# Optimization experiments

Hardware: AMD Instinct MI355X
Metric: run time of the kernel (lower is better)

The kernel has to match this reference:

```python
import jax, jax.numpy as jnp
import numpy as np

N_NODES = 50000
N_EDGES = 1000000


def _edge_conv(x, src, dst, W, b, n_nodes):
    """PyG EdgeConv: msg = nn(cat([x_i, x_j - x_i])), aggr=max over incoming edges."""
    xi = x[dst]                      # [E, C] target features
    xj = x[src]                      # [E, C] source features
    m = jnp.concatenate([xi, xj - xi], axis=-1)          # [E, 2C]
    m = jax.nn.relu(m @ W + b)                           # [E, C_out]
    out = jax.ops.segment_max(m, dst, num_segments=n_nodes)  # [N, C_out]
    # empty segments produce -inf; PyG fills with 0
    return jnp.where(jnp.isfinite(out), out, 0.0)


def setup_inputs() -> dict:
    key = jax.random.key(0)
    ks = jax.random.split(key, 12)
    x = jax.random.normal(ks[0], (N_NODES, 3), dtype=jnp.float32)
    edge_index = jax.random.randint(ks[1], (2, N_EDGES), 0, N_NODES, dtype=jnp.int64)

    def lin(k, fan_in, fan_out):
        s = 1.0 / np.sqrt(fan_in)
        kw, kb = jax.random.split(k)
        W = jax.random.uniform(kw, (fan_in, fan_out), jnp.float32, -s, s)
        b = jax.random.uniform(kb, (fan_out,), jnp.float32, -s, s)
        return W, b

    W1, b1 = lin(ks[2], 6, 64)       # conv1 MLP([3*2, 64])
    W2, b2 = lin(ks[3], 128, 128)    # conv2 MLP([64*2, 128])
    W3, b3 = lin(ks[4], 256, 512)    # conv3 MLP([128*2, 512])
    W4, b4 = lin(ks[5], 512, 256)    # lin1 MLP([512, 256])
    W5, b5 = lin(ks[6], 256, 3)      # lin1 final Linear(256, 3)
    return {"x": x, "edge_index": edge_index,
            "W1": W1, "b1": b1, "W2": W2, "b2": b2, "W3": W3, "b3": b3,
            "W4": W4, "b4": b4, "W5": W5, "b5": b5}


def reference(x, edge_index, W1, b1, W2, b2, W3, b3, W4, b4, W5, b5):
    src = edge_index[0]  # x_j
    dst = edge_index[1]  # x_i (aggregation target)
    n = x.shape[0]
    x1 = _edge_conv(x, src, dst, W1, b1, n)    # [N, 64]
    x2 = _edge_conv(x1, src, dst, W2, b2, n)   # [N, 128]
    x3 = _edge_conv(x2, src, dst, W3, b3, n)   # [N, 512]
    x4 = jax.nn.relu(x3 @ W4 + b4) @ W5 + b5   # [N, 3]
    return x + x4
```

## Files before the change

kernel.cpp:

```cpp
#include <hip/hip_runtime.h>

static constexpr int NN = 50000;
static constexpr int NE = 1000000;

typedef short bf16x8 __attribute__((ext_vector_type(8)));
typedef float f32x4 __attribute__((ext_vector_type(4)));
typedef unsigned short u16x2 __attribute__((ext_vector_type(2)));

__device__ inline float bf2f_raw(unsigned short u) {
    return __uint_as_float(((unsigned int)u) << 16);
}
__device__ inline unsigned short f2bf(float f) {
    unsigned int u = __float_as_uint(f);
    u += 0x7fffu + ((u >> 16) & 1u);
    return (unsigned short)(u >> 16);
}
__device__ inline unsigned short f2bfs(float f) {
    unsigned short b = f2bf(f);
    return (b & 0x8000u) ? (unsigned short)(~b) : (unsigned short)(b | 0x8000u);
}
__device__ inline float unsrt2f(unsigned short v) {
    unsigned short b = (v & 0x8000u) ? (unsigned short)(v ^ 0x8000u)
                                     : (unsigned short)(~v);
    return bf2f_raw(b);
}
__device__ inline unsigned int pkmax(unsigned int a, unsigned int b) {
    u16x2 r = __builtin_elementwise_max(__builtin_bit_cast(u16x2, a),
                                        __builtin_bit_cast(u16x2, b));
    return __builtin_bit_cast(unsigned int, r);
}
__device__ inline uint4 pkmax4(uint4 a, uint4 b) {
    a.x = pkmax(a.x, b.x); a.y = pkmax(a.y, b.y);
    a.z = pkmax(a.z, b.z); a.w = pkmax(a.w, b.w);
    return a;
}
__device__ inline unsigned int pack2(float f0, float f1) {
    return (unsigned int)f2bf(f0) | ((unsigned int)f2bf(f1) << 16);
}
__device__ inline unsigned int addrelu2t(unsigned int a, unsigned int t) {
    float t0 = unsrt2f((unsigned short)(t & 0xffffu));
    float t1 = unsrt2f((unsigned short)(t >> 16));
    float f0 = fmaxf(bf2f_raw((unsigned short)(a & 0xffffu)) + t0, 0.f);
    float f1 = fmaxf(bf2f_raw((unsigned short)(a >> 16)) + t1, 0.f);
    return pack2(f0, f1);
}


__global__ void setup_kernel(const float* __restrict__ x, const float* __restrict__ W1,
                             const float* __restrict__ b1, const float* __restrict__ b5,
                             const float* __restrict__ W2, const float* __restrict__ W3,
                             const float* __restrict__ W4,
                             unsigned short* __restrict__ as1, float* __restrict__ out,
                             int* __restrict__ deg, int* __restrict__ cursor,
                             unsigned short* __restrict__ Bt2,
                             unsigned short* __restrict__ Bt3,
                             unsigned short* __restrict__ W4t) {
    int t = blockIdx.x * blockDim.x + threadIdx.x;
    if (t < NN * 128) {
        int i = t >> 7, c = t & 127;
        float x0 = x[i * 3 + 0], x1 = x[i * 3 + 1], x2 = x[i * 3 + 2];
        if (c < 64) {
            float v = x0 * (W1[c] - W1[192 + c]) + x1 * (W1[64 + c] - W1[256 + c]) +
                      x2 * (W1[128 + c] - W1[320 + c]) + b1[c];
            as1[t] = f2bf(v);
        } else {
            int cs = c - 64;
            float v = x0 * W1[192 + cs] + x1 * W1[256 + cs] + x2 * W1[320 + cs];
            as1[t] = f2bfs(v);
        }
        return;
    }
    t -= NN * 128;
    if (t < NN * 3) { out[t] = x[t] + b5[t % 3]; return; }
    t -= NN * 3;
    if (t < NN) { deg[t] = 0; return; }
    t -= NN;
    if (t < NN) { cursor[t] = 0; return; }
    t -= NN;
    if (t < 8192) {
        int k = t / 128, c = t % 128;
        float wt = W2[k * 128 + c];
        float wb = W2[(64 + k) * 128 + c];
        Bt2[c * 64 + k] = f2bf(wt - wb);
        Bt2[(128 + c) * 64 + k] = f2bf(wb);
        return;
    }
    t -= 8192;
    if (t < 65536) {
        int k = t / 512, c = t % 512;
        float wt = W3[k * 512 + c];
        float wb = W3[(128 + k) * 512 + c];
        Bt3[c * 128 + k] = f2bf(wt - wb);
        Bt3[(512 + c) * 128 + k] = f2bf(wb);
        return;
    }
    t -= 65536;
    if (t < 131072) {
        int k = t / 256, n = t % 256;
        W4t[n * 512 + k] = f2bf(W4[k * 256 + n]);
    }
}


__global__ void hist_kernel(const int* __restrict__ dst, int* __restrict__ deg) {
    int e = blockIdx.x * blockDim.x + threadIdx.x;
    if (e < NE) atomicAdd(&deg[dst[e]], 1);
}

__global__ __launch_bounds__(1024) void scan_kernel(const int* __restrict__ deg,
                                                    int* __restrict__ rowstart) {
    __shared__ int wave_sums[16];
    constexpr int CH = (NN + 1023) / 1024;
    int tid = threadIdx.x;
    int lane = tid & 63;
    int wave = tid >> 6;
    int base = tid * CH;
    int vals[CH];
    int sum = 0;
    #pragma unroll
    for (int i = 0; i < CH; ++i) {
        int idx = base + i;
        vals[i] = (idx < NN) ? deg[idx] : 0;
        sum += vals[i];
    }
    int x = sum;
    #pragma unroll
    for (int off = 1; off < 64; off <<= 1) {
        int y = __shfl_up(x, off);
        if (lane >= off) x += y;
    }
    if (lane == 63) wave_sums[wave] = x;
    __syncthreads();
    if (wave == 0 && lane < 16) {
        int s = wave_sums[lane];
        #pragma unroll
        for (int off = 1; off < 16; off <<= 1) {
            int y = __shfl_up(s, off);
            if (lane >= off) s += y;
        }
        wave_sums[lane] = s;
    }
    __syncthreads();
    int run = (wave ? wave_sums[wave - 1] : 0) + x - sum;
    #pragma unroll
    for (int i = 0; i < CH; ++i) {
        int idx = base + i;
        if (idx < NN) rowstart[idx] = run;
        run += vals[i];
    }
    if (tid == 1023) rowstart[NN] = run;
}

__global__ void scatter_kernel(const int* __restrict__ src, const int* __restrict__ dst,
                               const int* __restrict__ rowstart, int* __restrict__ cursor,
                               int* __restrict__ csr) {
    int e = blockIdx.x * blockDim.x + threadIdx.x;
    if (e < NE) {
        int d = dst[e];
        int pos = atomicAdd(&cursor[d], 1);
        csr[rowstart[d] + pos] = src[e];
    }
}


__global__ __launch_bounds__(256) void edge_fused_conv1_kernel(
    const unsigned short* __restrict__ as, const int* __restrict__ rowstart,
    const int* __restrict__ csr, unsigned short* __restrict__ x1) {
    int wid = (blockIdx.x * 256 + threadIdx.x) >> 6;
    int lane = threadIdx.x & 63;
    if (wid >= NN) return;
    int e0 = __builtin_amdgcn_readfirstlane(rowstart[wid]);
    int e1 = __builtin_amdgcn_readfirstlane(rowstart[wid + 1]);
    int nedge = e1 - e0;
    unsigned int mA = 0u, mB = 0u;
    if (nedge > 0) {
        int last = nedge - 1;
        for (int e = 0; e < nedge; e += 16) {
            int jj[16];
            #pragma unroll
            for (int k = 0; k < 16; ++k) {
                int idx = e + k; if (idx > last) idx = last;
                jj[k] = __builtin_amdgcn_readfirstlane(csr[e0 + idx]);
            }
            unsigned int v[16];
            #pragma unroll
            for (int k = 0; k < 16; ++k)
                v[k] = *(const unsigned short*)(as + (size_t)jj[k] * 128 + 64 + lane);
            #pragma unroll
            for (int k = 0; k < 16; ++k) {
                if (k & 1) mB = mB > v[k] ? mB : v[k];
                else       mA = mA > v[k] ? mA : v[k];
            }
        }
    }
    unsigned int m = mA > mB ? mA : mB;
    unsigned short a = as[(size_t)wid * 128 + lane];
    float t = unsrt2f((unsigned short)m);
    float f = fmaxf(bf2f_raw(a) + t, 0.f);
    x1[(size_t)wid * 64 + lane] = f2bf(f);
}


__global__ __launch_bounds__(256) void edge_fused128_kernel(
    const unsigned short* __restrict__ as, const int* __restrict__ rowstart,
    const int* __restrict__ csr, unsigned short* __restrict__ xout) {
    int wid = (blockIdx.x * 256 + threadIdx.x) >> 6;
    int lane = threadIdx.x & 63;
    if (wid >= NN) return;
    int e0 = __builtin_amdgcn_readfirstlane(rowstart[wid]);
    int e1 = __builtin_amdgcn_readfirstlane(rowstart[wid + 1]);
    int nedge = e1 - e0;
    unsigned int mA = 0u, mB = 0u;
    if (nedge > 0) {
        int last = nedge - 1;
        for (int e = 0; e < nedge; e += 16) {
            int jj[16];
            #pragma unroll
            for (int k = 0; k < 16; ++k) {
                int idx = e + k; if (idx > last) idx = last;
                jj[k] = __builtin_amdgcn_readfirstlane(csr[e0 + idx]);
            }
            unsigned int v[16];
            #pragma unroll
            for (int k = 0; k < 16; ++k)
                v[k] = *(const unsigned int*)(as + (size_t)jj[k] * 256 + 128 + lane * 2);
            #pragma unroll
            for (int k = 0; k < 16; ++k) {
                if (k & 1) mB = pkmax(mB, v[k]);
                else       mA = pkmax(mA, v[k]);
            }
        }
    }
    unsigned int t = pkmax(mA, mB);
    unsigned int av = *(const unsigned int*)(as + (size_t)wid * 256 + lane * 2);
    *(unsigned int*)(xout + (size_t)wid * 128 + lane * 2) = addrelu2t(av, t);
}


__global__ __launch_bounds__(256) void ef512_w5_kernel(
    const unsigned short* __restrict__ s3, const unsigned short* __restrict__ x2,
    const int* __restrict__ rowstart, const int* __restrict__ csr,
    const unsigned short* __restrict__ Bt3a, const float* __restrict__ b3,
    const unsigned short* __restrict__ W4t,
    const float* __restrict__ b4, const float* __restrict__ W5,
    float* __restrict__ out) {
    __shared__ __align__(16) unsigned short X[16][520];
    __shared__ __align__(16) unsigned short x2t[16][136];
    int tid = threadIdx.x;
    int wave = tid >> 6, lane = tid & 63;
    int quad = lane >> 4, l16 = lane & 15;
    int tilebase = blockIdx.x * 16;

    {
        int row = tid >> 4, seg = tid & 15;
        uint4 v = *(const uint4*)(x2 + (size_t)(tilebase + row) * 128 + seg * 8);
        *(uint4*)&x2t[row][seg * 8] = v;
    }
    __syncthreads();

    {
        int colbase = wave * 128;
        f32x4 acc3[8] = {};
        #pragma unroll
        for (int kc = 0; kc < 4; ++kc) {
            bf16x8 afr = *(const bf16x8*)&x2t[l16][kc * 32 + quad * 8];
            #pragma unroll
            for (int nt = 0; nt < 8; ++nt) {
                int col = colbase + nt * 16 + l16;
                bf16x8 bfr = *(const bf16x8*)&Bt3a[(size_t)col * 128 + kc * 32 + quad * 8];
                acc3[nt] = __builtin_amdgcn_mfma_f32_16x16x32_bf16(afr, bfr, acc3[nt], 0, 0, 0);
            }
        }
        #pragma unroll
        for (int nt = 0; nt < 8; ++nt) {
            int col = colbase + nt * 16 + l16;
            float bv = b3[col];
            #pragma unroll
            for (int r = 0; r < 4; ++r)
                X[quad * 4 + r][col] = f2bf(acc3[nt][r] + bv);
        }
    }
    __syncthreads();

    const unsigned short* sb = s3 + (size_t)lane * 8;
    for (int i = 0; i < 4; ++i) {
        int node = tilebase + wave * 4 + i;
        int e0 = __builtin_amdgcn_readfirstlane(rowstart[node]);
        int e1 = __builtin_amdgcn_readfirstlane(rowstart[node + 1]);
        int nedge = e1 - e0;
        uint4 mA = make_uint4(0u, 0u, 0u, 0u), mB = make_uint4(0u, 0u, 0u, 0u);
        if (nedge > 0) {
            int last = nedge - 1;
            for (int e = 0; e < nedge; e += 8) {
                int jj[8];
                #pragma unroll
                for (int k = 0; k < 8; ++k) {
                    int idx = e + k; if (idx > last) idx = last;
                    jj[k] = __builtin_amdgcn_readfirstlane(csr[e0 + idx]);
                }
                uint4 v[8];
                #pragma unroll
                for (int k = 0; k < 8; ++k)
                    v[k] = *(const uint4*)(sb + (size_t)jj[k] * 512);
                #pragma unroll
                for (int k = 0; k < 8; ++k) {
                    if (k & 1) mB = pkmax4(mB, v[k]);
                    else       mA = pkmax4(mA, v[k]);
                }
            }
        }
        uint4 m = pkmax4(mA, mB);
        uint4 av = *(const uint4*)&X[wave * 4 + i][lane * 8];
        uint4 o;
        o.x = addrelu2t(av.x, m.x);
        o.y = addrelu2t(av.y, m.y);
        o.z = addrelu2t(av.z, m.z);
        o.w = addrelu2t(av.w, m.w);
        *(uint4*)&X[wave * 4 + i][lane * 8] = o;
    }
    __syncthreads();

    int colbase = wave * 64;
    f32x4 acc4[4] = {};
    for (int kc = 0; kc < 16; ++kc) {
        bf16x8 afr = *(const bf16x8*)&X[l16][kc * 32 + quad * 8];
        #pragma unroll
        for (int nt = 0; nt < 4; ++nt) {
            int col = colbase + nt * 16 + l16;
            bf16x8 bfr = *(const bf16x8*)&W4t[(size_t)col * 512 + kc * 32 + quad * 8];
            acc4[nt] = __builtin_amdgcn_mfma_f32_16x16x32_bf16(afr, bfr, acc4[nt], 0, 0, 0);
        }
    }
    float b4v[4], w5r[4][3];
    #pragma unroll
    for (int nt = 0; nt < 4; ++nt) {
        int col = colbase + nt * 16 + l16;
        b4v[nt] = b4[col];
        w5r[nt][0] = W5[col * 3 + 0];
        w5r[nt][1] = W5[col * 3 + 1];
        w5r[nt][2] = W5[col * 3 + 2];
    }
    #pragma unroll
    for (int r = 0; r < 4; ++r) {
        int row = tilebase + quad * 4 + r;
        float p0 = 0.f, p1 = 0.f, p2 = 0.f;
        #pragma unroll
        for (int nt = 0; nt < 4; ++nt) {
            float h = fmaxf(acc4[nt][r] + b4v[nt], 0.f);
            p0 += h * w5r[nt][0];
            p1 += h * w5r[nt][1];
            p2 += h * w5r[nt][2];
        }
        #pragma unroll
        for (int m = 8; m; m >>= 1) {
            p0 += __shfl_xor(p0, m);
            p1 += __shfl_xor(p1, m);
            p2 += __shfl_xor(p2, m);
        }
        if (l16 == 0) {
            atomicAdd(&out[row * 3 + 0], p0);
            atomicAdd(&out[row * 3 + 1], p1);
            atomicAdd(&out[row * 3 + 2], p2);
        }
    }
}


template<int K, int NT>
__global__ __launch_bounds__(256) void mfma_gemm_nloop_kernel(
    const unsigned short* __restrict__ A, const unsigned short* __restrict__ Bt,
    const float* __restrict__ bias, int bias_n,
    unsigned short* __restrict__ C, int M) {
    constexpr int KC = K / 32;
    constexpr int N = NT * 128;
    __shared__ __align__(16) unsigned short Asl[KC][128 * 40];
    __shared__ __align__(16) unsigned short Bsl[128 * 40];
    int tid = threadIdx.x;
    int mbase = blockIdx.x * 128;
    int wave = tid >> 6, lane = tid & 63;
    int wm = (wave >> 1) * 64, wn = (wave & 1) * 64;
    int quad = lane >> 4, l16 = lane & 15;

    #pragma unroll
    for (int c = tid; c < KC * 512; c += 256) {
        int kc = c >> 9, rem = c & 511;
        int r = rem >> 2, kk = (rem & 3) * 8;
        uint4 va = make_uint4(0u, 0u, 0u, 0u);
        int gr = mbase + r;
        if (gr < M) va = *(const uint4*)&A[(size_t)gr * K + kc * 32 + kk];
        *(uint4*)&Asl[kc][r * 40 + kk] = va;
    }

    for (int nt = 0; nt < NT; ++nt) {
        int nbase = nt * 128;
        f32x4 acc[4][4] = {};
        for (int kc = 0; kc < KC; ++kc) {
            __syncthreads();
            #pragma unroll
            for (int h = 0; h < 2; ++h) {
                int c = tid + h * 256;
                int r = c >> 2, kk = (c & 3) * 8;
                uint4 vb = *(const uint4*)&Bt[(size_t)(nbase + r) * K + kc * 32 + kk];
                *(uint4*)&Bsl[r * 40 + kk] = vb;
            }
            __syncthreads();
            bf16x8 af[4], bfr[4];
            #pragma unroll
            for (int tt = 0; tt < 4; ++tt) {
                af[tt]  = *(const bf16x8*)&Asl[kc][(wm + tt * 16 + l16) * 40 + quad * 8];
                bfr[tt] = *(const bf16x8*)&Bsl[(wn + tt * 16 + l16) * 40 + quad * 8];
            }
            #pragma unroll
            for (int mt = 0; mt < 4; ++mt)
                #pragma unroll
                for (int ntt = 0; ntt < 4; ++ntt)
                    acc[mt][ntt] = __builtin_amdgcn_mfma_f32_16x16x32_bf16(
                        af[mt], bfr[ntt], acc[mt][ntt], 0, 0, 0);
        }
        #pragma unroll
        for (int mt = 0; mt < 4; ++mt) {
            #pragma unroll
            for (int r = 0; r < 4; ++r) {
                int row = mbase + wm + mt * 16 + quad * 4 + r;
                if (row >= M) continue;
                #pragma unroll
                for (int ntt = 0; ntt < 4; ++ntt) {
                    int col = nbase + wn + ntt * 16 + l16;
                    float v = acc[mt][ntt][r];
                    unsigned short o;
                    if (col < bias_n) o = f2bf(v + bias[col]);
                    else o = f2bfs(v);
                    C[(size_t)row * N + col] = o;
                }
            }
        }
    }
}

__global__ void fallback_copy_kernel(const float* __restrict__ x, float* __restrict__ out) {
    int t = blockIdx.x * blockDim.x + threadIdx.x;
    if (t < NN * 3) out[t] = x[t];
}


extern "C" void kernel_launch(void* const* d_in, const int* in_sizes, int n_in,
                              void* d_out, int out_size, void* d_ws, size_t ws_size,
                              hipStream_t stream) {
    const float* x  = (const float*)d_in[0];
    const int*   ei = (const int*)d_in[1];
    const float* W1 = (const float*)d_in[2];
    const float* b1 = (const float*)d_in[3];
    const float* W2 = (const float*)d_in[4];
    const float* b2 = (const float*)d_in[5];
    const float* W3 = (const float*)d_in[6];
    const float* b3 = (const float*)d_in[7];
    const float* W4 = (const float*)d_in[8];
    const float* b4 = (const float*)d_in[9];
    const float* W5 = (const float*)d_in[10];
    const float* b5 = (const float*)d_in[11];
    float* out = (float*)d_out;

    char* p = (char*)d_ws;
    auto alloc = [&](size_t bytes) -> void* {
        void* r = (void*)p;
        p += (bytes + 255) & ~(size_t)255;
        return r;
    };
    int* deg      = (int*)alloc((size_t)NN * 4);
    int* rowstart = (int*)alloc((size_t)(NN + 1) * 4);
    int* cursor   = (int*)alloc((size_t)NN * 4);
    int* csr      = (int*)alloc((size_t)NE * 4);
    unsigned short* Bt2 = (unsigned short*)alloc(256 * 64 * 2);
    unsigned short* Bt3 = (unsigned short*)alloc(1024 * 128 * 2);
    unsigned short* W4t = (unsigned short*)alloc(256 * 512 * 2);
    unsigned short* x1 = (unsigned short*)alloc((size_t)NN * 64 * 2);
    unsigned short* x2 = (unsigned short*)alloc((size_t)NN * 128 * 2);
    unsigned short* as_slab = (unsigned short*)alloc((size_t)NN * 512 * 2);
    size_t need = (size_t)(p - (char*)d_ws);
    if (ws_size < need) {
        fallback_copy_kernel<<<(NN * 3 + 255) / 256, 256, 0, stream>>>(x, out);
        return;
    }

    const int* src = ei;
    const int* dst = ei + NE;

    constexpr int SETUP_T = NN * 128 + NN * 3 + NN + NN + 8192 + 65536 + 131072;
    setup_kernel<<<(SETUP_T + 255) / 256, 256, 0, stream>>>(
        x, W1, b1, b5, W2, W3, W4, as_slab, out, deg, cursor, Bt2, Bt3, W4t);

    hist_kernel<<<(NE + 255) / 256, 256, 0, stream>>>(dst, deg);
    scan_kernel<<<1, 1024, 0, stream>>>(deg, rowstart);
    scatter_kernel<<<(NE + 255) / 256, 256, 0, stream>>>(src, dst, rowstart, cursor, csr);

    edge_fused_conv1_kernel<<<12500, 256, 0, stream>>>(as_slab, rowstart, csr, x1);

    mfma_gemm_nloop_kernel<64, 2><<<391, 256, 0, stream>>>(
        x1, Bt2, b2, 128, as_slab, NN);
    edge_fused128_kernel<<<12500, 256, 0, stream>>>(as_slab, rowstart, csr, x2);

    mfma_gemm_nloop_kernel<128, 4><<<391, 256, 0, stream>>>(
        x2, Bt3 + 512 * 128, b3, 0, as_slab, NN);

    ef512_w5_kernel<<<NN / 16, 256, 0, stream>>>(
        as_slab, x2, rowstart, csr, Bt3, b3, W4t, b4, W5, out);
}
```

Measured before the change: 580.3 us.

## Fuse conv2 self-term GEMM into edge max kernel and reorder conv3 tile work

The conv2 GEMM now computes only the neighbour half (128 columns) into a compact slab. The per-node self term (x1·W_a + b) is computed inside a new tiled edge-max kernel with MFMA on a 16-node tile, so the slab stride for the gathered neighbour rows drops from 256 to 128 shorts. In the conv3 kernel the gather/max runs before the self-term MFMA, with the A fragments preloaded from shared memory, so gather latency and MFMA work can overlap across waves. This trades a smaller gathered slab and less GEMM output traffic for extra per-block MFMA work and registers holding the max results.

```diff
diff --git a/kernel.cpp b/kernel.cpp
--- a/kernel.cpp
+++ b/kernel.cpp
@@ -201,39 +201,86 @@
 }
 
 
-__global__ __launch_bounds__(256) void edge_fused128_kernel(
-    const unsigned short* __restrict__ as, const int* __restrict__ rowstart,
-    const int* __restrict__ csr, unsigned short* __restrict__ xout) {
-    int wid = (blockIdx.x * 256 + threadIdx.x) >> 6;
-    int lane = threadIdx.x & 63;
-    if (wid >= NN) return;
-    int e0 = __builtin_amdgcn_readfirstlane(rowstart[wid]);
-    int e1 = __builtin_amdgcn_readfirstlane(rowstart[wid + 1]);
-    int nedge = e1 - e0;
-    unsigned int mA = 0u, mB = 0u;
-    if (nedge > 0) {
-        int last = nedge - 1;
-        for (int e = 0; e < nedge; e += 16) {
-            int jj[16];
-            #pragma unroll
-            for (int k = 0; k < 16; ++k) {
-                int idx = e + k; if (idx > last) idx = last;
-                jj[k] = __builtin_amdgcn_readfirstlane(csr[e0 + idx]);
-            }
-            unsigned int v[16];
-            #pragma unroll
-            for (int k = 0; k < 16; ++k)
-                v[k] = *(const unsigned int*)(as + (size_t)jj[k] * 256 + 128 + lane * 2);
-            #pragma unroll
-            for (int k = 0; k < 16; ++k) {
-                if (k & 1) mB = pkmax(mB, v[k]);
-                else       mA = pkmax(mA, v[k]);
-            }
-        }
-    }
-    unsigned int t = pkmax(mA, mB);
-    unsigned int av = *(const unsigned int*)(as + (size_t)wid * 256 + lane * 2);
-    *(unsigned int*)(xout + (size_t)wid * 128 + lane * 2) = addrelu2t(av, t);
+__global__ __launch_bounds__(256) void ef128_a2_kernel(
+    const unsigned short* __restrict__ s2, const unsigned short* __restrict__ x1,
+    const int* __restrict__ rowstart, const int* __restrict__ csr,
+    const unsigned short* __restrict__ Bt2a, const float* __restrict__ b2,
+    unsigned short* __restrict__ x2) {
+    __shared__ __align__(16) unsigned short x1t[16][72];
+    __shared__ __align__(16) unsigned short A2[16][136];
+    int tid = threadIdx.x;
+    int wave = tid >> 6, lane = tid & 63;
+    int quad = lane >> 4, l16 = lane & 15;
+    int tilebase = blockIdx.x * 16;
+
+    if (tid < 128) {
+        int row = tid >> 3, seg = tid & 7;
+        uint4 v = *(const uint4*)(x1 + (size_t)(tilebase + row) * 64 + seg * 8);
+        *(uint4*)&x1t[row][seg * 8] = v;
+    }
+    __syncthreads();
+
+    unsigned int m[4];
+    for (int i = 0; i < 4; ++i) {
+        int node = tilebase + wave * 4 + i;
+        int e0 = __builtin_amdgcn_readfirstlane(rowstart[node]);
+        int e1 = __builtin_amdgcn_readfirstlane(rowstart[node + 1]);
+        int nedge = e1 - e0;
+        unsigned int mA = 0u, mB = 0u;
+        if (nedge > 0) {
+            int last = nedge - 1;
+            for (int e = 0; e < nedge; e += 16) {
+                int jj[16];
+                #pragma unroll
+                for (int k = 0; k < 16; ++k) {
+                    int idx = e + k; if (idx > last) idx = last;
+                    jj[k] = __builtin_amdgcn_readfirstlane(csr[e0 + idx]);
+                }
+                unsigned int v[16];
+                #pragma unroll
+                for (int k = 0; k < 16; ++k)
+                    v[k] = *(const unsigned int*)(s2 + (size_t)jj[k] * 128 + lane * 2);
+                #pragma unroll
+                for (int k = 0; k < 16; ++k) {
+                    if (k & 1) mB = pkmax(mB, v[k]);
+                    else       mA = pkmax(mA, v[k]);
+                }
+            }
+        }
+        m[i] = pkmax(mA, mB);
+    }
+
+    {
+        int colbase = wave * 32;
+        f32x4 acc[2] = {};
+        #pragma unroll
+        for (int kc = 0; kc < 2; ++kc) {
+            bf16x8 afr = *(const bf16x8*)&x1t[l16][kc * 32 + quad * 8];
+            #pragma unroll
+            for (int nt = 0; nt < 2; ++nt) {
+                int col = colbase + nt * 16 + l16;
+                bf16x8 bfr = *(const bf16x8*)&Bt2a[(size_t)col * 64 + kc * 32 + quad * 8];
+                acc[nt] = __builtin_amdgcn_mfma_f32_16x16x32_bf16(afr, bfr, acc[nt], 0, 0, 0);
+            }
+        }
+        #pragma unroll
+        for (int nt = 0; nt < 2; ++nt) {
+            int col = colbase + nt * 16 + l16;
+            float bv = b2[col];
+            #pragma unroll
+            for (int r = 0; r < 4; ++r)
+                A2[quad * 4 + r][col] = f2bf(acc[nt][r] + bv);
+        }
+    }
+    __syncthreads();
+
+    #pragma unroll
+    for (int i = 0; i < 4; ++i) {
+        int row = wave * 4 + i;
+        unsigned int av = *(const unsigned int*)&A2[row][lane * 2];
+        *(unsigned int*)(x2 + (size_t)(tilebase + row) * 128 + lane * 2) =
+            addrelu2t(av, m[i]);
+    }
 }
 
 
@@ -245,7 +292,6 @@
     const float* __restrict__ b4, const float* __restrict__ W5,
     float* __restrict__ out) {
     __shared__ __align__(16) unsigned short X[16][520];
-    __shared__ __align__(16) unsigned short x2t[16][136];
     int tid = threadIdx.x;
     int wave = tid >> 6, lane = tid & 63;
     int quad = lane >> 4, l16 = lane & 15;
@@ -254,35 +300,16 @@
     {
         int row = tid >> 4, seg = tid & 15;
         uint4 v = *(const uint4*)(x2 + (size_t)(tilebase + row) * 128 + seg * 8);
-        *(uint4*)&x2t[row][seg * 8] = v;
-    }
-    __syncthreads();
-
-    {
-        int colbase = wave * 128;
-        f32x4 acc3[8] = {};
-        #pragma unroll
-        for (int kc = 0; kc < 4; ++kc) {
-            bf16x8 afr = *(const bf16x8*)&x2t[l16][kc * 32 + quad * 8];
-            #pragma unroll
-            for (int nt = 0; nt < 8; ++nt) {
-                int col = colbase + nt * 16 + l16;
-                bf16x8 bfr = *(const bf16x8*)&Bt3a[(size_t)col * 128 + kc * 32 + quad * 8];
-                acc3[nt] = __builtin_amdgcn_mfma_f32_16x16x32_bf16(afr, bfr, acc3[nt], 0, 0, 0);
-            }
-        }
-        #pragma unroll
-        for (int nt = 0; nt < 8; ++nt) {
-            int col = colbase + nt * 16 + l16;
-            float bv = b3[col];
-            #pragma unroll
-            for (int r = 0; r < 4; ++r)
-                X[quad * 4 + r][col] = f2bf(acc3[nt][r] + bv);
-        }
-    }
-    __syncthreads();
-
-    const unsigned short* sb = s3 + (size_t)lane * 8;
+        *(uint4*)&X[row][seg * 8] = v;
+    }
+    __syncthreads();
+    bf16x8 afr[4];
+    #pragma unroll
+    for (int kc = 0; kc < 4; ++kc)
+        afr[kc] = *(const bf16x8*)&X[l16][kc * 32 + quad * 8];
+    __syncthreads();
+
+    uint4 m[4];
     for (int i = 0; i < 4; ++i) {
         int node = tilebase + wave * 4 + i;
         int e0 = __builtin_amdgcn_readfirstlane(rowstart[node]);
@@ -301,7 +328,7 @@
                 uint4 v[8];
                 #pragma unroll
                 for (int k = 0; k < 8; ++k)
-                    v[k] = *(const uint4*)(sb + (size_t)jj[k] * 512);
+                    v[k] = *(const uint4*)(s3 + (size_t)jj[k] * 512 + lane * 8);
                 #pragma unroll
                 for (int k = 0; k < 8; ++k) {
                     if (k & 1) mB = pkmax4(mB, v[k]);
@@ -309,26 +336,54 @@
                 }
             }
         }
-        uint4 m = pkmax4(mA, mB);
-        uint4 av = *(const uint4*)&X[wave * 4 + i][lane * 8];
+        m[i] = pkmax4(mA, mB);
+    }
+
+    {
+        int colbase = wave * 128;
+        f32x4 acc3[8] = {};
+        #pragma unroll
+        for (int kc = 0; kc < 4; ++kc) {
+            #pragma unroll
+            for (int nt = 0; nt < 8; ++nt) {
+                int col = colbase + nt * 16 + l16;
+                bf16x8 bfr = *(const bf16x8*)&Bt3a[(size_t)col * 128 + kc * 32 + quad * 8];
+                acc3[nt] = __builtin_amdgcn_mfma_f32_16x16x32_bf16(afr[kc], bfr, acc3[nt], 0, 0, 0);
+            }
+        }
+        #pragma unroll
+        for (int nt = 0; nt < 8; ++nt) {
+            int col = colbase + nt * 16 + l16;
+            float bv = b3[col];
+            #pragma unroll
+            for (int r = 0; r < 4; ++r)
+                X[quad * 4 + r][col] = f2bf(acc3[nt][r] + bv);
+        }
+    }
+    __syncthreads();
+
+    #pragma unroll
+    for (int i = 0; i < 4; ++i) {
+        int row = wave * 4 + i;
+        uint4 av = *(const uint4*)&X[row][lane * 8];
         uint4 o;
-        o.x = addrelu2t(av.x, m.x);
-        o.y = addrelu2t(av.y, m.y);
-        o.z = addrelu2t(av.z, m.z);
-        o.w = addrelu2t(av.w, m.w);
-        *(uint4*)&X[wave * 4 + i][lane * 8] = o;
+        o.x = addrelu2t(av.x, m[i].x);
+        o.y = addrelu2t(av.y, m[i].y);
+        o.z = addrelu2t(av.z, m[i].z);
+        o.w = addrelu2t(av.w, m[i].w);
+        *(uint4*)&X[row][lane * 8] = o;
     }
     __syncthreads();
 
     int colbase = wave * 64;
     f32x4 acc4[4] = {};
     for (int kc = 0; kc < 16; ++kc) {
-        bf16x8 afr = *(const bf16x8*)&X[l16][kc * 32 + quad * 8];
+        bf16x8 a4 = *(const bf16x8*)&X[l16][kc * 32 + quad * 8];
         #pragma unroll
         for (int nt = 0; nt < 4; ++nt) {
             int col = colbase + nt * 16 + l16;
             bf16x8 bfr = *(const bf16x8*)&W4t[(size_t)col * 512 + kc * 32 + quad * 8];
-            acc4[nt] = __builtin_amdgcn_mfma_f32_16x16x32_bf16(afr, bfr, acc4[nt], 0, 0, 0);
+            acc4[nt] = __builtin_amdgcn_mfma_f32_16x16x32_bf16(a4, bfr, acc4[nt], 0, 0, 0);
         }
     }
     float b4v[4], w5r[4][3];
@@ -352,10 +407,10 @@
             p2 += h * w5r[nt][2];
         }
         #pragma unroll
-        for (int m = 8; m; m >>= 1) {
-            p0 += __shfl_xor(p0, m);
-            p1 += __shfl_xor(p1, m);
-            p2 += __shfl_xor(p2, m);
+        for (int mm = 8; mm; mm >>= 1) {
+            p0 += __shfl_xor(p0, mm);
+            p1 += __shfl_xor(p1, mm);
+            p2 += __shfl_xor(p2, mm);
         }
         if (l16 == 0) {
             atomicAdd(&out[row * 3 + 0], p0);
@@ -495,9 +550,10 @@
 
     edge_fused_conv1_kernel<<<12500, 256, 0, stream>>>(as_slab, rowstart, csr, x1);
 
-    mfma_gemm_nloop_kernel<64, 2><<<391, 256, 0, stream>>>(
-        x1, Bt2, b2, 128, as_slab, NN);
-    edge_fused128_kernel<<<12500, 256, 0, stream>>>(as_slab, rowstart, csr, x2);
+    mfma_gemm_nloop_kernel<64, 1><<<391, 256, 0, stream>>>(
+        x1, Bt2 + 128 * 64, b2, 0, as_slab, NN);
+    ef128_a2_kernel<<<NN / 16, 256, 0, stream>>>(
+        as_slab, x1, rowstart, csr, Bt2, b2, x2);
 
     mfma_gemm_nloop_kernel<128, 4><<<391, 256, 0, stream>>>(
         x2, Bt3 + 512 * 128, b3, 0, as_slab, NN);
```

Result: no change. 579.0 us (-0.2%).
